# Performance work log

Hardware: AMD Instinct MI355X
Metric: run time of the kernel (lower is better)

Reference implementation:

```python
import jax, jax.numpy as jnp
import numpy as np

BATCH, FIELD, EMB = 2048, 32, 64
LAYER_SIZES = [64, 64, 64]
OUT_DIM = 1
FINAL_DIM = sum(LAYER_SIZES)  # 192 (direct_connect=True, no splits)


def setup_inputs() -> dict:
    key = jax.random.key(0)
    ks = jax.random.split(key, 10)
    inp = {
        "x0": jax.random.normal(ks[0], (BATCH, FIELD, EMB), dtype=jnp.float32),
        # Conv1d(kernel_size=1) weights reshaped to (out, prev_field, field):
        "W1": jax.random.normal(ks[1], (LAYER_SIZES[0], FIELD, FIELD), dtype=jnp.float32) * 0.05,
        "b1": jax.random.normal(ks[2], (LAYER_SIZES[0],), dtype=jnp.float32) * 0.05,
        "W2": jax.random.normal(ks[3], (LAYER_SIZES[1], LAYER_SIZES[0], FIELD), dtype=jnp.float32) * 0.05,
        "b2": jax.random.normal(ks[4], (LAYER_SIZES[1],), dtype=jnp.float32) * 0.05,
        "W3": jax.random.normal(ks[5], (LAYER_SIZES[2], LAYER_SIZES[1], FIELD), dtype=jnp.float32) * 0.05,
        "b3": jax.random.normal(ks[6], (LAYER_SIZES[2],), dtype=jnp.float32) * 0.05,
        "W_out": jax.random.normal(ks[7], (FINAL_DIM, OUT_DIM), dtype=jnp.float32) * 0.05,
        "b_out": jax.random.normal(ks[8], (OUT_DIM,), dtype=jnp.float32) * 0.05,
    }
    return inp


def _cin_layer(W, b, xk, x0):
    # Fused: outer product einsum('bhd,bmd->bhmd') + reshape + 1x1 conv
    # == einsum over (prev_field h, field m) channel pair, per emb dim d.
    return jnp.einsum("ohm,bhd,bmd->bod", W, xk, x0) + b[None, :, None]


def reference(x0, W1, b1, W2, b2, W3, b3, W_out, b_out):
    # activation = identity; direct_connect = True (no splits, full carry)
    h1 = _cin_layer(W1, b1, x0, x0)   # (B, 64, D)
    h2 = _cin_layer(W2, b2, h1, x0)   # (B, 64, D)
    h3 = _cin_layer(W3, b3, h2, x0)   # (B, 64, D)
    stacked = jnp.concatenate([h1, h2, h3], axis=1)  # (B, 192, D)
    pooled = stacked.sum(axis=2)                     # (B, 192)
    return pooled @ W_out + b_out                    # (B, 1)
```

## Files before the change

### kernel.cpp

```cpp
#include <hip/hip_runtime.h>

typedef _Float16 f16;
typedef _Float16 f16x2 __attribute__((ext_vector_type(2)));
typedef __fp16 fp16x2 __attribute__((ext_vector_type(2)));
typedef _Float16 f16x8 __attribute__((ext_vector_type(8)));
typedef float f32x4 __attribute__((ext_vector_type(4)));
typedef unsigned int u32;

union U2 { u32 u; f16x2 h; fp16x2 h2; };
union AF { f16x8 v; u32 u[4]; };

__global__ __launch_bounds__(256) void pre_all(
    const float* __restrict__ W1, const float* __restrict__ b1,
    const float* __restrict__ W2, const float* __restrict__ b2,
    const float* __restrict__ W3, const float* __restrict__ b3,
    const float* __restrict__ W_out, const float* __restrict__ b_out,
    f16* __restrict__ Wfrag, float* __restrict__ rvec, float* __restrict__ cnst) {
    const int blk = blockIdx.x, t = threadIdx.x;
    if (blk < 64) {
        const int h = blk;
        __shared__ float w3e[2048];
        __shared__ float w2s[2048];
        __shared__ float wo2[64];
#pragma unroll
        for (int i = 0; i < 8; ++i) {
            int idx = t + 256 * i;
            w2s[idx] = W2[((idx >> 5) * 64 + h) * 32 + (idx & 31)];
            float s = 0.f;
            for (int o3 = 0; o3 < 64; ++o3)
                s += W_out[128 + o3] * W3[o3 * 2048 + idx];
            w3e[idx] = s;
        }
        if (t < 64) wo2[t] = W_out[64 + t];
        __syncthreads();
        for (int idx = t; idx < 576; idx += 256) {
            int c = idx >> 5, kk = idx & 31;
            int sg = c >> 1, par = c & 1, A = kk >> 1, z = kk & 1;
            int B = (A + sg) & 15;
            float val = 0.f;
            if (sg == 0 && par == 1 && z == 1) {
                val = 0.f;
            } else if (sg == 8 && A >= 8) {
                int m = par ? (kk - 16) : kk;
                float s = 0.f;
                for (int o = 0; o < 64; ++o) s += wo2[o] * w2s[o * 32 + m];
                val = s;
            } else {
                int a = 2 * A + (par ? (1 - z) : z);
                int bq = 2 * B + z;
                float s = 0.f;
                if (a == bq) {
                    for (int o = 0; o < 64; ++o)
                        s += w3e[o * 32 + a] * w2s[o * 32 + a];
                } else {
                    for (int o = 0; o < 64; ++o)
                        s += w3e[o * 32 + bq] * w2s[o * 32 + a] +
                             w3e[o * 32 + a] * w2s[o * 32 + bq];
                }
                val = s;
            }
            int g = (kk >> 2) & 3, bb = (kk & 3) + 4 * (kk >> 4);
            int t4 = 4 + (h >> 4), l = 16 * g + (h & 15);
            Wfrag[((c * 8 + t4) * 64 + l) * 8 + bb] = (f16)val;
        }
    } else if (blk < 128) {
        const int h = blk - 64;
        __shared__ float w1r[1024];
        for (int i = t; i < 1024; i += 256) w1r[i] = W1[h * 1024 + i];
        __syncthreads();
        for (int idx = t; idx < 576; idx += 256) {
            int c = idx >> 5, kk = idx & 31;
            int sg = c >> 1, par = c & 1, A = kk >> 1, z = kk & 1;
            int B = (A + sg) & 15;
            float val = 0.f;
            if ((sg == 0 && par == 1 && z == 1) || (sg == 8 && A >= 8)) {
                val = 0.f;
            } else {
                int a = 2 * A + (par ? (1 - z) : z);
                int bq = 2 * B + z;
                val = (a == bq) ? w1r[33 * a] : (w1r[32 * a + bq] + w1r[32 * bq + a]);
            }
            int g = (kk >> 2) & 3, bb = (kk & 3) + 4 * (kk >> 4);
            int t4 = h >> 4, l = 16 * g + (h & 15);
            Wfrag[((c * 8 + t4) * 64 + l) * 8 + bb] = (f16)val;
        }
    } else {
        __shared__ float part[256];
        int m = t & 31, og = t >> 5;
        float s = 0.f;
        for (int oo = 0; oo < 8; ++oo) {
            int o = og * 8 + oo;
            float ah = 0.f;
            for (int hh = 0; hh < 64; ++hh)
                ah += b2[hh] * W3[(o * 64 + hh) * 32 + m];
            s += W_out[128 + o] * ah;
        }
        part[t] = s;
        __syncthreads();
        if (t < 32) {
            float r = 0.f;
#pragma unroll
            for (int og2 = 0; og2 < 8; ++og2) r += part[og2 * 32 + t];
            rvec[t] = r;
        }
        if (t == 32) {
            float s2 = 0.f;
            for (int o = 0; o < 64; ++o)
                s2 += b1[o] * W_out[o] + b2[o] * W_out[64 + o] + b3[o] * W_out[128 + o];
            cnst[0] = b_out[0] + 64.f * s2;
        }
    }
}


#define EPOS(row, col) ((row) * 64 + (((col) + 4 * (row)) & 63))

__global__ __launch_bounds__(256, 3) void cin_main(
    const float* __restrict__ x0, const f16* __restrict__ Wfrag,
    const float* __restrict__ b1, const float* __restrict__ W_out,
    const float* __restrict__ rvec, const float* __restrict__ cnst,
    float* __restrict__ out) {
    __shared__ __align__(16) u32 FQ[2 * 32 * 130];
    __shared__ float eps[2][16 * 64];
    __shared__ float b1s[64], w1s[64], rs[32], rvb[2], obuf[2][2];

    const int t = threadIdx.x;
    const int w = t >> 6, lane = t & 63;
    const int wr = w >> 1, wc = w & 1;
    const int g = (lane >> 4) & 3, l15 = lane & 15;
    const int blk = blockIdx.x;

    {
        const float* src = x0 + (size_t)blk * 4096;
        const int J = t >> 4, l = t & 15;
        int r0 = 2 * J, r1 = 2 * J + 1, r2 = (2 * J + 2) & 31, r3 = (2 * J + 3) & 31;
#pragma unroll
        for (int bl = 0; bl < 2; ++bl) {
            const float* sb = src + bl * 2048;
#pragma unroll
            for (int k2 = 0; k2 < 4; ++k2) {
                int d = 16 * k2 + l;
                U2 u0, u1;
                u0.h2 = __builtin_amdgcn_cvt_pkrtz(sb[r0 * 64 + d], sb[r1 * 64 + d]);
                u1.h2 = __builtin_amdgcn_cvt_pkrtz(sb[r2 * 64 + d], sb[r3 * 64 + d]);
                uint2 ent; ent.x = u0.u; ent.y = u1.u;
                int base = bl * 4160 + J * 130 + 2 * d;
                *reinterpret_cast<uint2*>(&FQ[base]) = ent;
                *reinterpret_cast<uint2*>(&FQ[base + 2080]) = ent;
            }
        }
    }
    if (t < 64) { b1s[t] = b1[t]; w1s[t] = W_out[t]; }
    if (t >= 64 && t < 96) rs[t - 64] = rvec[t - 64];
    __syncthreads();

    const int v1base = wr * 4160 + 260 * g + 2 * l15;

    U2 xp[4][4], xpsw[4][4];
#pragma unroll
    for (int s = 0; s < 4; ++s) {
        uint2 qa = *reinterpret_cast<const uint2*>(&FQ[v1base + 32 * s]);
        uint2 qb = *reinterpret_cast<const uint2*>(&FQ[v1base + 32 * s + 1040]);
        xp[s][0].u = qa.x; xp[s][1].u = qa.y; xp[s][2].u = qb.x; xp[s][3].u = qb.y;
#pragma unroll
        for (int i = 0; i < 4; ++i)
            xpsw[s][i].u = (xp[s][i].u >> 16) | (xp[s][i].u << 16);
    }

    f32x4 acc[4][4];
#pragma unroll
    for (int s = 0; s < 4; ++s)
#pragma unroll
        for (int tt = 0; tt < 4; ++tt) acc[s][tt] = f32x4{0.f, 0.f, 0.f, 0.f};

    const f16x8* Wg = reinterpret_cast<const f16x8*>(Wfrag);
    f16x8 bfA[4], bfB[4];
#pragma unroll
    for (int tt = 0; tt < 4; ++tt) bfA[tt] = Wg[(wc * 4 + tt) * 64 + lane];

#define PKU(xa, ub) ({ U2 b_; b_.u = (ub); U2 r_; r_.h = (xa).h * b_.h; r_.u; })

#define PREF(dst, cc) { _Pragma("unroll") for (int tt = 0; tt < 4; ++tt) \
    dst[tt] = Wg[((cc) * 8 + wc * 4 + tt) * 64 + lane]; }

#define BODY(cc, bfr) { \
    _Pragma("unroll") \
    for (int s = 0; s < 4; ++s) { \
        AF af; \
        if ((cc) == 0) { \
            _Pragma("unroll") \
            for (int i = 0; i < 4; ++i) af.u[i] = PKU(xp[s][i], xp[s][i].u); \
        } else if ((cc) == 1) { \
            _Pragma("unroll") \
            for (int i = 0; i < 4; ++i) af.u[i] = PKU(xpsw[s][i], xp[s][i].u); \
        } else if ((cc) < 16) { \
            uint2 qa = *reinterpret_cast<const uint2*>(&FQ[v1base + 32 * s + ((cc) >> 1) * 130]); \
            uint2 qb = *reinterpret_cast<const uint2*>(&FQ[v1base + 32 * s + 1040 + ((cc) >> 1) * 130]); \
            if ((cc) & 1) { \
                af.u[0] = PKU(xpsw[s][0], qa.x); af.u[1] = PKU(xpsw[s][1], qa.y); \
                af.u[2] = PKU(xpsw[s][2], qb.x); af.u[3] = PKU(xpsw[s][3], qb.y); \
            } else { \
                af.u[0] = PKU(xp[s][0], qa.x); af.u[1] = PKU(xp[s][1], qa.y); \
                af.u[2] = PKU(xp[s][2], qb.x); af.u[3] = PKU(xp[s][3], qb.y); \
            } \
        } else if ((cc) == 16) { \
            uint2 qa = *reinterpret_cast<const uint2*>(&FQ[v1base + 32 * s + 1040]); \
            af.u[0] = PKU(xp[s][0], qa.x); af.u[1] = PKU(xp[s][1], qa.y); \
            af.u[2] = xp[s][2].u; af.u[3] = xp[s][3].u; \
        } else { \
            uint2 qa = *reinterpret_cast<const uint2*>(&FQ[v1base + 32 * s + 1040]); \
            af.u[0] = PKU(xpsw[s][0], qa.x); af.u[1] = PKU(xpsw[s][1], qa.y); \
            af.u[2] = xp[s][0].u; af.u[3] = xp[s][1].u; \
        } \
        __builtin_amdgcn_s_setprio(1); \
        _Pragma("unroll") \
        for (int tt = 0; tt < 4; ++tt) \
            acc[s][tt] = __builtin_amdgcn_mfma_f32_16x16x32_f16(af.v, bfr[tt], acc[s][tt], 0, 0, 0); \
        __builtin_amdgcn_s_setprio(0); \
    } }

    PREF(bfB, 1);  BODY(0, bfA);
    PREF(bfA, 2);  BODY(1, bfB);
    PREF(bfB, 3);  BODY(2, bfA);
    PREF(bfA, 4);  BODY(3, bfB);
    PREF(bfB, 5);  BODY(4, bfA);
    PREF(bfA, 6);  BODY(5, bfB);
    PREF(bfB, 7);  BODY(6, bfA);
    PREF(bfA, 8);  BODY(7, bfB);
    PREF(bfB, 9);  BODY(8, bfA);
    PREF(bfA, 10); BODY(9, bfB);
    PREF(bfB, 11); BODY(10, bfA);
    PREF(bfA, 12); BODY(11, bfB);
    PREF(bfB, 13); BODY(12, bfA);
    PREF(bfA, 14); BODY(13, bfB);
    PREF(bfB, 15); BODY(14, bfA);
    PREF(bfA, 16); BODY(15, bfB);
    PREF(bfB, 17); BODY(16, bfA);
    BODY(17, bfB);

#undef BODY
#undef PREF
#undef PKU

    if (wc == 0) {
        float sum = 0.f;
#pragma unroll
        for (int J = 0; J < 16; ++J) {
            U2 v; v.u = FQ[wr * 4160 + J * 130 + 2 * lane];
            sum += rs[2 * J] * (float)v.h[0] + rs[2 * J + 1] * (float)v.h[1];
        }
#pragma unroll
        for (int off = 32; off; off >>= 1) sum += __shfl_xor(sum, off);
        if (lane == 0) rvb[wr] = sum;
    }

    float bs = 0.f;
#pragma unroll
    for (int s = 0; s < 4; ++s) {
        if (wc == 1) {
#pragma unroll
            for (int tt = 0; tt < 4; ++tt) {
                float w1v = w1s[16 * tt + l15];
                float b1v = b1s[16 * tt + l15];
#pragma unroll
                for (int r = 0; r < 4; ++r) {
                    float a = acc[s][tt][r];
                    eps[wr][EPOS(4 * g + r, 16 * tt + l15)] = a + w1v;
                    bs += b1v * a;
                }
            }
        }
        __syncthreads();
        if (wc == 0) {
#pragma unroll
            for (int tt = 0; tt < 4; ++tt)
#pragma unroll
                for (int r = 0; r < 4; ++r)
                    bs += acc[s][tt][r] * eps[wr][EPOS(4 * g + r, 16 * tt + l15)];
        }
        __syncthreads();
    }
#pragma unroll
    for (int off = 32; off; off >>= 1) bs += __shfl_xor(bs, off);
    if (lane == 0) obuf[wr][wc] = bs;
    __syncthreads();
    if (t < 2)
        out[blk * 2 + t] = cnst[0] + rvb[t] + obuf[t][0] + obuf[t][1];
}

extern "C" void kernel_launch(void* const* d_in, const int* in_sizes, int n_in,
                              void* d_out, int out_size, void* d_ws, size_t ws_size,
                              hipStream_t stream) {
    const float* x0    = (const float*)d_in[0];
    const float* W1    = (const float*)d_in[1];
    const float* b1    = (const float*)d_in[2];
    const float* W2    = (const float*)d_in[3];
    const float* b2    = (const float*)d_in[4];
    const float* W3    = (const float*)d_in[5];
    const float* b3    = (const float*)d_in[6];
    const float* W_out = (const float*)d_in[7];
    const float* b_out = (const float*)d_in[8];

    char* wsb = (char*)d_ws;
    f16*   Wfrag = (f16*)wsb;
    float* rvecp = (float*)(wsb + 147456);
    float* cnstp = rvecp + 32;
    float* outp  = (float*)d_out;

    hipLaunchKernelGGL(pre_all,  dim3(129),  dim3(256), 0, stream,
                       W1, b1, W2, b2, W3, b3, W_out, b_out, Wfrag, rvecp, cnstp);
    hipLaunchKernelGGL(cin_main, dim3(1024), dim3(256), 0, stream,
                       x0, Wfrag, b1, W_out, rvecp, cnstp, outp);
}
```

Baseline: 45.60 us.

## Hoist W3·W_out contraction into a separate kernel shared by all blocks

The W_out-weighted contraction of W3 was previously recomputed in each of 64 preprocessing blocks with long serial loops; it now runs once in a small dedicated kernel and the result is read from workspace. The rvec and constant terms are rederived from this shared result and a wave shuffle reduction, shortening their serial chains. This adds one extra kernel launch and a global round-trip for the intermediate.

```diff
diff --git a/kernel.cpp b/kernel.cpp
--- a/kernel.cpp
+++ b/kernel.cpp
@@ -10,11 +10,29 @@
 union U2 { u32 u; f16x2 h; fp16x2 h2; };
 union AF { f16x8 v; u32 u[4]; };
 
-__global__ __launch_bounds__(256) void pre_all(
+__global__ __launch_bounds__(256) void pre_w3eff(
+    const float* __restrict__ W3, const float* __restrict__ W_out,
+    float* __restrict__ W3eff) {
+    const int idx = blockIdx.x * 256 + threadIdx.x;
+    float acc[8] = {0.f, 0.f, 0.f, 0.f, 0.f, 0.f, 0.f, 0.f};
+#pragma unroll
+    for (int ob = 0; ob < 8; ++ob)
+#pragma unroll
+        for (int oi = 0; oi < 8; ++oi) {
+            int o = ob * 8 + oi;
+            acc[oi] += W_out[128 + o] * W3[o * 2048 + idx];
+        }
+    float s = 0.f;
+#pragma unroll
+    for (int oi = 0; oi < 8; ++oi) s += acc[oi];
+    W3eff[idx] = s;
+}
+
+__global__ __launch_bounds__(256) void pre_rest(
     const float* __restrict__ W1, const float* __restrict__ b1,
     const float* __restrict__ W2, const float* __restrict__ b2,
-    const float* __restrict__ W3, const float* __restrict__ b3,
-    const float* __restrict__ W_out, const float* __restrict__ b_out,
+    const float* __restrict__ b3, const float* __restrict__ W_out,
+    const float* __restrict__ b_out, const float* __restrict__ W3eff_g,
     f16* __restrict__ Wfrag, float* __restrict__ rvec, float* __restrict__ cnst) {
     const int blk = blockIdx.x, t = threadIdx.x;
     if (blk < 64) {
@@ -25,11 +43,8 @@
 #pragma unroll
         for (int i = 0; i < 8; ++i) {
             int idx = t + 256 * i;
+            w3e[idx] = W3eff_g[idx];
             w2s[idx] = W2[((idx >> 5) * 64 + h) * 32 + (idx & 31)];
-            float s = 0.f;
-            for (int o3 = 0; o3 < 64; ++o3)
-                s += W_out[128 + o3] * W3[o3 * 2048 + idx];
-            w3e[idx] = s;
         }
         if (t < 64) wo2[t] = W_out[64 + t];
         __syncthreads();
@@ -43,6 +58,7 @@
             } else if (sg == 8 && A >= 8) {
                 int m = par ? (kk - 16) : kk;
                 float s = 0.f;
+#pragma unroll 8
                 for (int o = 0; o < 64; ++o) s += wo2[o] * w2s[o * 32 + m];
                 val = s;
             } else {
@@ -50,9 +66,11 @@
                 int bq = 2 * B + z;
                 float s = 0.f;
                 if (a == bq) {
+#pragma unroll 8
                     for (int o = 0; o < 64; ++o)
                         s += w3e[o * 32 + a] * w2s[o * 32 + a];
                 } else {
+#pragma unroll 8
                     for (int o = 0; o < 64; ++o)
                         s += w3e[o * 32 + bq] * w2s[o * 32 + a] +
                              w3e[o * 32 + a] * w2s[o * 32 + bq];
@@ -85,29 +103,27 @@
             Wfrag[((c * 8 + t4) * 64 + l) * 8 + bb] = (f16)val;
         }
     } else {
-        __shared__ float part[256];
-        int m = t & 31, og = t >> 5;
-        float s = 0.f;
-        for (int oo = 0; oo < 8; ++oo) {
-            int o = og * 8 + oo;
-            float ah = 0.f;
-            for (int hh = 0; hh < 64; ++hh)
-                ah += b2[hh] * W3[(o * 64 + hh) * 32 + m];
-            s += W_out[128 + o] * ah;
-        }
-        part[t] = s;
-        __syncthreads();
         if (t < 32) {
+            float acc[8] = {0.f, 0.f, 0.f, 0.f, 0.f, 0.f, 0.f, 0.f};
+#pragma unroll
+            for (int hb = 0; hb < 8; ++hb)
+#pragma unroll
+                for (int hi = 0; hi < 8; ++hi) {
+                    int h = hb * 8 + hi;
+                    acc[hi] += b2[h] * W3eff_g[h * 32 + t];
+                }
             float r = 0.f;
 #pragma unroll
-            for (int og2 = 0; og2 < 8; ++og2) r += part[og2 * 32 + t];
+            for (int hi = 0; hi < 8; ++hi) r += acc[hi];
             rvec[t] = r;
         }
-        if (t == 32) {
-            float s2 = 0.f;
-            for (int o = 0; o < 64; ++o)
-                s2 += b1[o] * W_out[o] + b2[o] * W_out[64 + o] + b3[o] * W_out[128 + o];
-            cnst[0] = b_out[0] + 64.f * s2;
+        if (t >= 64 && t < 128) {
+            int o = t - 64;
+            float v = b1[o] * W_out[o] + b2[o] * W_out[64 + o] +
+                      b3[o] * W_out[128 + o];
+#pragma unroll
+            for (int off = 32; off; off >>= 1) v += __shfl_xor(v, off);
+            if (o == 0) cnst[0] = b_out[0] + 64.f * v;
         }
     }
 }
@@ -303,12 +319,14 @@
 
     char* wsb = (char*)d_ws;
     f16*   Wfrag = (f16*)wsb;
-    float* rvecp = (float*)(wsb + 147456);
+    float* W3effp = (float*)(wsb + 147456);
+    float* rvecp = W3effp + 2048;
     float* cnstp = rvecp + 32;
     float* outp  = (float*)d_out;
 
-    hipLaunchKernelGGL(pre_all,  dim3(129),  dim3(256), 0, stream,
-                       W1, b1, W2, b2, W3, b3, W_out, b_out, Wfrag, rvecp, cnstp);
-    hipLaunchKernelGGL(cin_main, dim3(1024), dim3(256), 0, stream,
+    hipLaunchKernelGGL(pre_w3eff, dim3(8),   dim3(256), 0, stream, W3, W_out, W3effp);
+    hipLaunchKernelGGL(pre_rest,  dim3(129), dim3(256), 0, stream,
+                       W1, b1, W2, b2, b3, W_out, b_out, W3effp, Wfrag, rvecp, cnstp);
+    hipLaunchKernelGGL(cin_main,  dim3(1024), dim3(256), 0, stream,
                        x0, Wfrag, b1, W_out, rvecp, cnstp, outp);
 }
```

Result: faster. 40.81 us (-10.5%).
